# Performance work log

Hardware: AMD Instinct MI355X
Metric: run time of the kernel (lower is better)

The kernel has to match this reference:

```python
import jax, jax.numpy as jnp
import numpy as np

B, T, VOCAB = 8192, 1024, 10000

def setup_inputs() -> dict:
    key = jax.random.key(0)
    k1, k2, k3, k4 = jax.random.split(key, 4)
    sample_seq = jax.random.randint(k1, (B, T), 0, VOCAB, dtype=jnp.int32)
    sample_seqLogprobs = jax.random.normal(k2, (B, T), dtype=jnp.float32)
    sample_value = jax.random.normal(k3, (B, T), dtype=jnp.float32)
    sample_reward = jax.random.normal(k4, (B, T), dtype=jnp.float32)
    return {
        "sample_seq": sample_seq,
        "sample_seqLogprobs": sample_seqLogprobs,
        "sample_value": sample_value,
        "sample_reward": sample_reward,
    }

def reference(sample_seq, sample_seqLogprobs, sample_value, sample_reward):
    # Vectorized version of the per-element python loop: zero out every token
    # at or after the first EOS (token id 0). cumsum>0 of the EOS indicator is
    # the running-max (cummax) of (seq==0).
    at_or_after_eos = jnp.cumsum((sample_seq == 0).astype(jnp.int32), axis=1) > 0
    seq = jnp.where(at_or_after_eos, 0, sample_seq)  # [B, T]

    # mask = (seq>0), shifted right by one with a leading column of ones
    mask = (seq > 0).astype(sample_seqLogprobs.dtype)
    mask = jnp.concatenate(
        [jnp.ones((mask.shape[0], 1), mask.dtype), mask[:, :-1]], axis=1
    )

    # sample_reward is a detached numpy array in the original (no grad)
    reward = jax.lax.stop_gradient(sample_reward)
    reward_diff = reward - sample_value  # [B, T]

    # masked REINFORCE loss, normalized by number of valid tokens
    output = -sample_seqLogprobs * reward_diff * mask
    loss = output.sum() / mask.sum()
    return loss
```

## Files before the change

### kernel.cpp

```cpp
#include <hip/hip_runtime.h>

#define BROWS 8192
#define TLEN  1024

typedef float f32x4 __attribute__((ext_vector_type(4)));
typedef int   i32x4 __attribute__((ext_vector_type(4)));

__global__ __launch_bounds__(256) void row_reduce_kernel(
    const int*   __restrict__ seq,
    const float* __restrict__ logp,
    const float* __restrict__ value,
    const float* __restrict__ reward,
    float*       __restrict__ row_sum,
    float*       __restrict__ row_cnt)
{
    const int row  = blockIdx.x * 4 + (threadIdx.x >> 6);
    const int lane = threadIdx.x & 63;

    const size_t rowoff = (size_t)row * TLEN;
    const i32x4* s4 = (const i32x4*)(seq    + rowoff);
    const f32x4* l4 = (const f32x4*)(logp   + rowoff);
    const f32x4* v4 = (const f32x4*)(value  + rowoff);
    const f32x4* r4 = (const f32x4*)(reward + rowoff);

    i32x4 s[4];
    f32x4 l[4], v[4], r[4];
    #pragma unroll
    for (int k = 0; k < 4; ++k) {
        const int idx = k * 64 + lane;
        s[k] = __builtin_nontemporal_load(s4 + idx);
        l[k] = __builtin_nontemporal_load(l4 + idx);
        v[k] = __builtin_nontemporal_load(v4 + idx);
        r[k] = __builtin_nontemporal_load(r4 + idx);
    }

    int lfz = TLEN;
    #pragma unroll
    for (int k = 3; k >= 0; --k) {
        const int base = k * 256 + lane * 4;
        if (s[k][3] == 0) lfz = base + 3;
        if (s[k][2] == 0) lfz = base + 2;
        if (s[k][1] == 0) lfz = base + 1;
        if (s[k][0] == 0) lfz = base + 0;
    }

    int fz = lfz;
    #pragma unroll
    for (int off = 32; off > 0; off >>= 1)
        fz = min(fz, __shfl_xor(fz, off, 64));

    float a0 = 0.0f, a1 = 0.0f, a2 = 0.0f, a3 = 0.0f;
    #pragma unroll
    for (int k = 0; k < 4; ++k) {
        const int base = k * 256 + lane * 4;
        a0 += (base + 0 <= fz) ? (-l[k][0] * (r[k][0] - v[k][0])) : 0.0f;
        a1 += (base + 1 <= fz) ? (-l[k][1] * (r[k][1] - v[k][1])) : 0.0f;
        a2 += (base + 2 <= fz) ? (-l[k][2] * (r[k][2] - v[k][2])) : 0.0f;
        a3 += (base + 3 <= fz) ? (-l[k][3] * (r[k][3] - v[k][3])) : 0.0f;
    }
    float acc = (a0 + a1) + (a2 + a3);

    #pragma unroll
    for (int off = 32; off > 0; off >>= 1)
        acc += __shfl_xor(acc, off, 64);

    if (lane == 0) {
        row_sum[row] = acc;
        row_cnt[row] = (float)min(fz + 1, TLEN);
    }
}

__global__ __launch_bounds__(256) void final_reduce_kernel(
    const float* __restrict__ row_sum,
    const float* __restrict__ row_cnt,
    float*       __restrict__ out)
{
    const int tid  = threadIdx.x;
    const int lane = tid & 63;
    const int wave = tid >> 6;

    double s = 0.0, c = 0.0;
    for (int i = tid; i < BROWS; i += 256) {
        s += (double)row_sum[i];
        c += (double)row_cnt[i];
    }
    #pragma unroll
    for (int off = 32; off > 0; off >>= 1) {
        s += __shfl_xor(s, off, 64);
        c += __shfl_xor(c, off, 64);
    }
    __shared__ double ls[4], lc[4];
    if (lane == 0) { ls[wave] = s; lc[wave] = c; }
    __syncthreads();
    if (tid == 0) {
        double ts = (ls[0] + ls[1]) + (ls[2] + ls[3]);
        double tc = (lc[0] + lc[1]) + (lc[2] + lc[3]);
        out[0] = (float)(ts / tc);
    }
}

extern "C" void kernel_launch(void* const* d_in, const int* in_sizes, int n_in,
                              void* d_out, int out_size, void* d_ws, size_t ws_size,
                              hipStream_t stream) {
    const int*   seq    = (const int*)  d_in[0];
    const float* logp   = (const float*)d_in[1];
    const float* value  = (const float*)d_in[2];
    const float* reward = (const float*)d_in[3];
    float* out = (float*)d_out;

    float* row_sum = (float*)d_ws;
    float* row_cnt = row_sum + BROWS;

    row_reduce_kernel<<<BROWS / 4, 256, 0, stream>>>(seq, logp, value, reward,
                                                     row_sum, row_cnt);
    final_reduce_kernel<<<1, 256, 0, stream>>>(row_sum, row_cnt, out);
}
```

Baseline: 147.6 us.

## Fuse final reduction into row kernel via global atomics and last-block finish

Removes the separate single-block final reduction kernel. Each block now reduces its four rows in shared memory, atomically adds its partial sum and count to global accumulators, and the last block to arrive (tracked by an atomic counter) computes the quotient. A memset clears the accumulators each call. The trade is one fewer kernel launch and no row buffer, against 2048-way float atomic contention, an extra memset node, and a non-deterministic float32 sum order replacing the double-precision final reduction.

```diff
diff --git a/kernel.cpp b/kernel.cpp
--- a/kernel.cpp
+++ b/kernel.cpp
@@ -2,20 +2,25 @@
 
 #define BROWS 8192
 #define TLEN  1024
+#define GRID  (BROWS / 4)
 
 typedef float f32x4 __attribute__((ext_vector_type(4)));
 typedef int   i32x4 __attribute__((ext_vector_type(4)));
+
 
 __global__ __launch_bounds__(256) void row_reduce_kernel(
     const int*   __restrict__ seq,
     const float* __restrict__ logp,
     const float* __restrict__ value,
     const float* __restrict__ reward,
-    float*       __restrict__ row_sum,
-    float*       __restrict__ row_cnt)
+    float*       __restrict__ sum_acc,
+    float*       __restrict__ cnt_acc,
+    int*         __restrict__ arrive,
+    float*       __restrict__ out)
 {
-    const int row  = blockIdx.x * 4 + (threadIdx.x >> 6);
+    const int wave = threadIdx.x >> 6;
     const int lane = threadIdx.x & 63;
+    const int row  = blockIdx.x * 4 + wave;
 
     const size_t rowoff = (size_t)row * TLEN;
     const i32x4* s4 = (const i32x4*)(seq    + rowoff);
@@ -64,38 +69,25 @@
     for (int off = 32; off > 0; off >>= 1)
         acc += __shfl_xor(acc, off, 64);
 
+    __shared__ float ls[4], lc[4];
     if (lane == 0) {
-        row_sum[row] = acc;
-        row_cnt[row] = (float)min(fz + 1, TLEN);
+        ls[wave] = acc;
+        lc[wave] = (float)min(fz + 1, TLEN);
     }
-}
+    __syncthreads();
 
-__global__ __launch_bounds__(256) void final_reduce_kernel(
-    const float* __restrict__ row_sum,
-    const float* __restrict__ row_cnt,
-    float*       __restrict__ out)
-{
-    const int tid  = threadIdx.x;
-    const int lane = tid & 63;
-    const int wave = tid >> 6;
-
-    double s = 0.0, c = 0.0;
-    for (int i = tid; i < BROWS; i += 256) {
-        s += (double)row_sum[i];
-        c += (double)row_cnt[i];
-    }
-    #pragma unroll
-    for (int off = 32; off > 0; off >>= 1) {
-        s += __shfl_xor(s, off, 64);
-        c += __shfl_xor(c, off, 64);
-    }
-    __shared__ double ls[4], lc[4];
-    if (lane == 0) { ls[wave] = s; lc[wave] = c; }
-    __syncthreads();
-    if (tid == 0) {
-        double ts = (ls[0] + ls[1]) + (ls[2] + ls[3]);
-        double tc = (lc[0] + lc[1]) + (lc[2] + lc[3]);
-        out[0] = (float)(ts / tc);
+    if (threadIdx.x == 0) {
+        const float bs = (ls[0] + ls[1]) + (ls[2] + ls[3]);
+        const float bc = (lc[0] + lc[1]) + (lc[2] + lc[3]);
+        atomicAdd(sum_acc, bs);
+        atomicAdd(cnt_acc, bc);
+        __threadfence();
+        const int old = atomicAdd(arrive, 1);
+        if (old == GRID - 1) {
+            const float ts = atomicAdd(sum_acc, 0.0f);
+            const float tc = atomicAdd(cnt_acc, 0.0f);
+            out[0] = ts / tc;
+        }
     }
 }
 
@@ -108,10 +100,11 @@
     const float* reward = (const float*)d_in[3];
     float* out = (float*)d_out;
 
-    float* row_sum = (float*)d_ws;
-    float* row_cnt = row_sum + BROWS;
+    float* sum_acc = (float*)d_ws;
+    float* cnt_acc = sum_acc + 1;
+    int*   arrive  = (int*)((char*)d_ws + 8);
 
-    row_reduce_kernel<<<BROWS / 4, 256, 0, stream>>>(seq, logp, value, reward,
-                                                     row_sum, row_cnt);
-    final_reduce_kernel<<<1, 256, 0, stream>>>(row_sum, row_cnt, out);
+    hipMemsetAsync(d_ws, 0, 16, stream);
+    row_reduce_kernel<<<GRID, 256, 0, stream>>>(seq, logp, value, reward,
+                                                sum_acc, cnt_acc, arrive, out);
 }
```

Result: slower. 240.9 us (+63.2%).
